# Kernel tuning notes

Hardware: AMD Instinct MI355X
Metric: run time of the kernel (lower is better)

The kernel has to match this reference:

```python
import jax, jax.numpy as jnp
import numpy as np

INV_SQRT2 = np.float32(1.0 / np.sqrt(2.0))


def _dwt1(x, axis):
    # pywt db1 (Haar), even-length: cA=(even+odd)/sqrt2, cD=(even-odd)/sqrt2
    ev = jax.lax.slice_in_dim(x, 0, None, 2, axis)
    od = jax.lax.slice_in_dim(x, 1, None, 2, axis)
    return (ev + od) * INV_SQRT2, (ev - od) * INV_SQRT2


def _idwt1(lo, hi, axis):
    ev = (lo + hi) * INV_SQRT2
    od = (lo - hi) * INV_SQRT2
    st = jnp.stack([ev, od], axis=axis + 1)  # (.., n, 2, ..)
    new_shape = list(lo.shape)
    new_shape[axis] *= 2
    return st.reshape(new_shape)


def haar_dwt2(x):
    lo, hi = _dwt1(x, 1)      # along width
    ll, lh = _dwt1(lo, 0)     # along height
    hl, hh = _dwt1(hi, 0)
    return ll, lh, hl, hh


def haar_idwt2(ll, lh, hl, hh):
    lo = _idwt1(ll, lh, 0)
    hi = _idwt1(hl, hh, 0)
    return _idwt1(lo, hi, 1)


def conv_same(img, w, b):
    # img: [h, w] -> 1x1-channel SAME conv with bias
    y = jax.lax.conv_general_dilated(
        img[None, None], w, (1, 1), 'SAME',
        dimension_numbers=('NCHW', 'OIHW', 'NCHW'))
    return y[0, 0] + b[0]


def setup_inputs() -> dict:
    key = jax.random.key(0)
    ks = jax.random.split(key, 7)
    H = W = 4096
    return {
        'x': jax.random.normal(ks[0], (1, 1, H, W), dtype=jnp.float32),
        'w3': jax.random.normal(ks[1], (1, 1, 3, 3), dtype=jnp.float32) * 0.1,
        'b3': jax.random.normal(ks[2], (1,), dtype=jnp.float32) * 0.1,
        'w5': jax.random.normal(ks[3], (1, 1, 5, 5), dtype=jnp.float32) * 0.1,
        'b5': jax.random.normal(ks[4], (1,), dtype=jnp.float32) * 0.1,
        'w7': jax.random.normal(ks[5], (1, 1, 7, 7), dtype=jnp.float32) * 0.1,
        'b7': jax.random.normal(ks[6], (1,), dtype=jnp.float32) * 0.1,
    }


def reference(x, w3, b3, w5, b5, w7, b7):
    img = x[0, 0]
    # 3-level wavedec2: collect details finest -> coarsest
    details = []
    cur = img
    for _ in range(3):
        ll, lh, hl, hh = haar_dwt2(cur)
        details.append((lh, hl, hh))
        cur = ll
    # pywt coeff order is coarsest-first, so in the torch code:
    # HH1 = coarsest (3x3), HH2 = mid (5x5), HH3 = finest (7x7)
    lh_c, hl_c, hh_c = details[2]
    lh_m, hl_m, hh_m = details[1]
    lh_f, hl_f, hh_f = details[0]
    hh_c = conv_same(hh_c, w3, b3)
    hh_m = conv_same(hh_m, w5, b5)
    hh_f = conv_same(hh_f, w7, b7)
    # waverec2: coarsest -> finest
    rec = haar_idwt2(cur, lh_c, hl_c, hh_c)
    rec = haar_idwt2(rec, lh_m, hl_m, hh_m)
    rec = haar_idwt2(rec, lh_f, hl_f, hh_f)
    return rec[None, None]
```

## Files before the change

### kernel.cpp

```cpp
#include <hip/hip_runtime.h>
#include <stddef.h>

#define IMG_N 4096

#define S_LH1   0
#define S_HL1   1680
#define S_HH1   3360
#define S_LL1   5040
#define S_HH1C  6720
#define S_LL2   7872
#define S_LH2   8272
#define S_HL2   8672
#define S_HH2   9072
#define S_LL2P  9472
#define S_LL3   9792
#define S_LH3   9892
#define S_HL3   9992
#define S_HH3   10092
#define S_TOTAL 10192

#define S_LL1P  (S_LL1)

__global__ __launch_bounds__(512, 8) void haar_fused(
    const float* __restrict__ x,
    const float* __restrict__ w3, const float* __restrict__ b3,
    const float* __restrict__ w5, const float* __restrict__ b5,
    const float* __restrict__ w7, const float* __restrict__ b7,
    float* __restrict__ out)
{
    __shared__ __align__(16) float sm[S_TOTAL];
    const int tid = threadIdx.x;
    const int bx = blockIdx.x, by = blockIdx.y;
    const int R0 = by * 64, C0 = bx * 64;

    float* LH1 = sm + S_LH1;
    float* HL1 = sm + S_HL1;
    float* HH1 = sm + S_HH1;
    float* LL1 = sm + S_LL1;
    float* HH1C = sm + S_HH1C;
    float* LL2 = sm + S_LL2;
    float* LH2 = sm + S_LH2;
    float* HL2 = sm + S_HL2;
    float* HH2 = sm + S_HH2;
    float* LL2P = sm + S_LL2P;
    float* LL3 = sm + S_LL3;
    float* LH3 = sm + S_LH3;
    float* HL3 = sm + S_HL3;
    float* HH3 = sm + S_HH3;
    float* LL1P = sm + S_LL1P;

    const bool interior = (by >= 1) && (by <= 62) && (bx >= 1) && (bx <= 62);
    if (interior) {
        const float* src = x + (size_t)(R0 - 8) * IMG_N + (C0 - 8);
        for (int idx = tid; idx < 800; idx += 512) {
            int u = idx / 20, v2 = (idx % 20) * 2;
            const float* p = src + (size_t)(2 * u) * IMG_N + 2 * v2;
            float4 t = *(const float4*)(p);
            float4 b = *(const float4*)(p + IMG_N);
            int o = u * 42 + v2;
            *(float2*)(LL1 + o) = make_float2((t.x + t.y + b.x + b.y) * 0.5f,
                                              (t.z + t.w + b.z + b.w) * 0.5f);
            *(float2*)(LH1 + o) = make_float2((t.x + t.y - b.x - b.y) * 0.5f,
                                              (t.z + t.w - b.z - b.w) * 0.5f);
            *(float2*)(HL1 + o) = make_float2((t.x - t.y + b.x - b.y) * 0.5f,
                                              (t.z - t.w + b.z - b.w) * 0.5f);
            *(float2*)(HH1 + o) = make_float2((t.x - t.y - b.x + b.y) * 0.5f,
                                              (t.z - t.w - b.z + b.w) * 0.5f);
        }
    } else {
        for (int idx = tid; idx < 800; idx += 512) {
            int u = idx / 20, v2 = (idx % 20) * 2;
            int gr0 = R0 - 8 + 2 * u, gr1 = gr0 + 1;
            int gc = C0 - 8 + 2 * v2;
            bool r0v = (gr0 >= 0 && gr0 < IMG_N), r1v = (gr1 >= 0 && gr1 < IMG_N);
            float tv[4], bv[4];
            #pragma unroll
            for (int k = 0; k < 4; ++k) {
                int g = gc + k;
                bool cv = (g >= 0 && g < IMG_N);
                tv[k] = (r0v && cv) ? x[(size_t)gr0 * IMG_N + g] : 0.0f;
                bv[k] = (r1v && cv) ? x[(size_t)gr1 * IMG_N + g] : 0.0f;
            }
            int o = u * 42 + v2;
            *(float2*)(LL1 + o) = make_float2((tv[0] + tv[1] + bv[0] + bv[1]) * 0.5f,
                                              (tv[2] + tv[3] + bv[2] + bv[3]) * 0.5f);
            *(float2*)(LH1 + o) = make_float2((tv[0] + tv[1] - bv[0] - bv[1]) * 0.5f,
                                              (tv[2] + tv[3] - bv[2] - bv[3]) * 0.5f);
            *(float2*)(HL1 + o) = make_float2((tv[0] - tv[1] + bv[0] - bv[1]) * 0.5f,
                                              (tv[2] - tv[3] + bv[2] - bv[3]) * 0.5f);
            *(float2*)(HH1 + o) = make_float2((tv[0] - tv[1] - bv[0] + bv[1]) * 0.5f,
                                              (tv[2] - tv[3] - bv[2] + bv[3]) * 0.5f);
        }
    }
    __syncthreads();

    if (tid < 256) {
        const int i = tid >> 3;
        const int j0 = (tid & 7) << 2;
        const float bias = b7[0];
        float a0 = bias, a1 = bias, a2 = bias, a3 = bias;
        #pragma unroll
        for (int dy = 0; dy < 7; ++dy) {
            const float* row = HH1 + (i + dy + 1) * 42 + (j0 + 1);
            const float* wr = w7 + dy * 7;
            float r0 = row[0], r1 = row[1], r2 = row[2], r3 = row[3], r4 = row[4],
                  r5 = row[5], r6 = row[6], r7 = row[7], r8 = row[8], r9 = row[9];
            float q0 = wr[0], q1 = wr[1], q2 = wr[2], q3 = wr[3], q4 = wr[4],
                  q5 = wr[5], q6 = wr[6];
            a0 += q0*r0 + q1*r1 + q2*r2 + q3*r3 + q4*r4 + q5*r5 + q6*r6;
            a1 += q0*r1 + q1*r2 + q2*r3 + q3*r4 + q4*r5 + q5*r6 + q6*r7;
            a2 += q0*r2 + q1*r3 + q2*r4 + q3*r5 + q4*r6 + q5*r7 + q6*r8;
            a3 += q0*r3 + q1*r4 + q2*r5 + q3*r6 + q4*r7 + q5*r8 + q6*r9;
        }
        *(float4*)(HH1C + i * 36 + j0) = make_float4(a0, a1, a2, a3);
    } else {
        int t = tid - 256;
        if (t < 200) {
            int u = t / 10, v2 = (t % 10) * 2;
            float4 tt = *(const float4*)(LL1 + (2 * u) * 42 + 2 * v2);
            float4 bb = *(const float4*)(LL1 + (2 * u + 1) * 42 + 2 * v2);
            int o = u * 20 + v2;
            *(float2*)(LL2 + o) = make_float2((tt.x + tt.y + bb.x + bb.y) * 0.5f,
                                              (tt.z + tt.w + bb.z + bb.w) * 0.5f);
            *(float2*)(LH2 + o) = make_float2((tt.x + tt.y - bb.x - bb.y) * 0.5f,
                                              (tt.z + tt.w - bb.z - bb.w) * 0.5f);
            *(float2*)(HL2 + o) = make_float2((tt.x - tt.y + bb.x - bb.y) * 0.5f,
                                              (tt.z - tt.w + bb.z - bb.w) * 0.5f);
            *(float2*)(HH2 + o) = make_float2((tt.x - tt.y - bb.x + bb.y) * 0.5f,
                                              (tt.z - tt.w - bb.z + bb.w) * 0.5f);
        }
    }
    __syncthreads();

    {
        int lane = tid & 63;
        if (lane < 50) {
            int u = lane / 5, v2 = (lane % 5) * 2;
            float4 tt = *(const float4*)(LL2 + (2 * u) * 20 + 2 * v2);
            float4 bb = *(const float4*)(LL2 + (2 * u + 1) * 20 + 2 * v2);
            int o = u * 10 + v2;
            *(float2*)(LL3 + o) = make_float2((tt.x + tt.y + bb.x + bb.y) * 0.5f,
                                              (tt.z + tt.w + bb.z + bb.w) * 0.5f);
            *(float2*)(LH3 + o) = make_float2((tt.x + tt.y - bb.x - bb.y) * 0.5f,
                                              (tt.z + tt.w - bb.z - bb.w) * 0.5f);
            *(float2*)(HL3 + o) = make_float2((tt.x - tt.y + bb.x - bb.y) * 0.5f,
                                              (tt.z - tt.w + bb.z - bb.w) * 0.5f);
            *(float2*)(HH3 + o) = make_float2((tt.x - tt.y - bb.x + bb.y) * 0.5f,
                                              (tt.z - tt.w - bb.z + bb.w) * 0.5f);
        }
        __builtin_amdgcn_wave_barrier();
        __builtin_amdgcn_s_waitcnt(0);
    }

    {
        const float b3c = b3[0];
        #pragma unroll
        for (int k = 0; k < 2; ++k) {
            int item = (tid & 63) + 64 * k;
            int p = item >> 3, c = item & 7;
            int r = p >> 1;
            float sr = (p & 1) ? -1.0f : 1.0f;
            float hh = b3c;
            #pragma unroll
            for (int dy = 0; dy < 3; ++dy) {
                const float* row = HH3 + (r + dy) * 10 + c;
                const float* wr = w3 + dy * 3;
                hh += wr[0]*row[0] + wr[1]*row[1] + wr[2]*row[2];
            }
            int li = (r + 1) * 10 + (c + 1);
            float lo = LL3[li] + sr * LH3[li];
            float hi = HL3[li] + sr * hh;
            *(float2*)(LL2P + p * 20 + 2 * c) =
                make_float2((lo + hi) * 0.5f, (lo - hi) * 0.5f);
        }
        __builtin_amdgcn_wave_barrier();
        __builtin_amdgcn_s_waitcnt(0);
    }

    {
        const float b5c = b5[0];
        int p = tid >> 4, c = tid & 15;
        int r = p >> 1;
        float sr = (p & 1) ? -1.0f : 1.0f;
        float hh = b5c;
        #pragma unroll
        for (int dy = 0; dy < 5; ++dy) {
            const float* row = HH2 + (r + dy) * 20 + c;
            const float* wr = w5 + dy * 5;
            hh += wr[0]*row[0] + wr[1]*row[1] + wr[2]*row[2] + wr[3]*row[3]
                + wr[4]*row[4];
        }
        int li = (r + 2) * 20 + (c + 2);
        float lo = LL2P[r * 20 + c] + sr * LH2[li];
        float hi = HL2[li] + sr * hh;
        *(float2*)(LL1P + p * 36 + 2 * c) =
            make_float2((lo + hi) * 0.5f, (lo - hi) * 0.5f);
    }
    __syncthreads();

    for (int idx = tid; idx < 1024; idx += 512) {
        const int p = idx >> 4;
        const int c2 = (idx & 15) * 2;
        const int r = p >> 1;
        const float sr = (p & 1) ? -1.0f : 1.0f;
        const int li = (r + 4) * 42 + (c2 + 4);
        const int ci = r * 36 + c2;
        float lo0 = LL1P[ci]     + sr * LH1[li];
        float hi0 = HL1[li]      + sr * HH1C[ci];
        float lo1 = LL1P[ci + 1] + sr * LH1[li + 1];
        float hi1 = HL1[li + 1]  + sr * HH1C[ci + 1];
        float4 o = make_float4((lo0 + hi0) * 0.5f, (lo0 - hi0) * 0.5f,
                               (lo1 + hi1) * 0.5f, (lo1 - hi1) * 0.5f);
        *(float4*)(out + (size_t)(R0 + p) * IMG_N + C0 + 2 * c2) = o;
    }
}

extern "C" void kernel_launch(void* const* d_in, const int* in_sizes, int n_in,
                              void* d_out, int out_size, void* d_ws, size_t ws_size,
                              hipStream_t stream) {
    (void)in_sizes; (void)n_in; (void)out_size; (void)d_ws; (void)ws_size;
    const float* x  = (const float*)d_in[0];
    const float* w3 = (const float*)d_in[1];
    const float* b3 = (const float*)d_in[2];
    const float* w5 = (const float*)d_in[3];
    const float* b5 = (const float*)d_in[4];
    const float* w7 = (const float*)d_in[5];
    const float* b7 = (const float*)d_in[6];
    float* out = (float*)d_out;

    dim3 grid(IMG_N / 64, IMG_N / 64);
    dim3 block(512);
    haar_fused<<<grid, block, 0, stream>>>(x, w3, b3, w5, b5, w7, b7, out);
}
```

Measured before the change: 142.3 us.

## Widen LDS rows to 44, vectorize Haar stages, precompute 5x5 conv, nontemporal stores

Pads first-level subband rows to 44 floats so every thread can load eight input columns with 2x float4 and write float4 results to LDS. The 7x7 conv reads rows as float4, and the level-2 split runs on 100 threads with float4 output. The 5x5 conv is moved into a separate stage that runs alongside the level-3 split, using shared-memory regions that are no longer needed. The final output is written with nontemporal stores. This adds one more __syncthreads and replaces the earlier wave-level barriers with block barriers.

```diff
diff --git a/kernel.cpp b/kernel.cpp
--- a/kernel.cpp
+++ b/kernel.cpp
@@ -3,23 +3,26 @@
 
 #define IMG_N 4096
 
+typedef float vf4 __attribute__((ext_vector_type(4)));
+
 #define S_LH1   0
-#define S_HL1   1680
-#define S_HH1   3360
-#define S_LL1   5040
-#define S_HH1C  6720
-#define S_LL2   7872
-#define S_LH2   8272
-#define S_HL2   8672
-#define S_HH2   9072
-#define S_LL2P  9472
-#define S_LL3   9792
-#define S_LH3   9892
-#define S_HL3   9992
-#define S_HH3   10092
-#define S_TOTAL 10192
-
+#define S_HL1   1760
+#define S_HH1   3520
+#define S_LL1   5280
+#define S_HH1C  7040
+#define S_LL2   8192
+#define S_LH2   8592
+#define S_HL2   8992
+#define S_HH2   9392
+#define S_TOTAL 9792
+
+#define S_HH2C  (S_HH1)
+#define S_LL3   (S_HH1 + 320)
+#define S_LH3   (S_HH1 + 420)
+#define S_HL3   (S_HH1 + 520)
+#define S_HH3   (S_HH1 + 620)
 #define S_LL1P  (S_LL1)
+#define S_LL2P  (S_LL1 + 1152)
 
 __global__ __launch_bounds__(512, 8) void haar_fused(
     const float* __restrict__ x,
@@ -33,64 +36,61 @@
     const int bx = blockIdx.x, by = blockIdx.y;
     const int R0 = by * 64, C0 = bx * 64;
 
-    float* LH1 = sm + S_LH1;
-    float* HL1 = sm + S_HL1;
-    float* HH1 = sm + S_HH1;
-    float* LL1 = sm + S_LL1;
+    float* LH1 = sm + S_LH1;   float* HL1 = sm + S_HL1;
+    float* HH1 = sm + S_HH1;   float* LL1 = sm + S_LL1;
     float* HH1C = sm + S_HH1C;
-    float* LL2 = sm + S_LL2;
-    float* LH2 = sm + S_LH2;
-    float* HL2 = sm + S_HL2;
-    float* HH2 = sm + S_HH2;
-    float* LL2P = sm + S_LL2P;
-    float* LL3 = sm + S_LL3;
-    float* LH3 = sm + S_LH3;
-    float* HL3 = sm + S_HL3;
-    float* HH3 = sm + S_HH3;
-    float* LL1P = sm + S_LL1P;
+    float* LL2 = sm + S_LL2;   float* LH2 = sm + S_LH2;
+    float* HL2 = sm + S_HL2;   float* HH2 = sm + S_HH2;
+    float* HH2C = sm + S_HH2C;
+    float* LL3 = sm + S_LL3;   float* LH3 = sm + S_LH3;
+    float* HL3 = sm + S_HL3;   float* HH3 = sm + S_HH3;
+    float* LL1P = sm + S_LL1P; float* LL2P = sm + S_LL2P;
 
     const bool interior = (by >= 1) && (by <= 62) && (bx >= 1) && (bx <= 62);
-    if (interior) {
-        const float* src = x + (size_t)(R0 - 8) * IMG_N + (C0 - 8);
-        for (int idx = tid; idx < 800; idx += 512) {
-            int u = idx / 20, v2 = (idx % 20) * 2;
-            const float* p = src + (size_t)(2 * u) * IMG_N + 2 * v2;
-            float4 t = *(const float4*)(p);
-            float4 b = *(const float4*)(p + IMG_N);
-            int o = u * 42 + v2;
-            *(float2*)(LL1 + o) = make_float2((t.x + t.y + b.x + b.y) * 0.5f,
-                                              (t.z + t.w + b.z + b.w) * 0.5f);
-            *(float2*)(LH1 + o) = make_float2((t.x + t.y - b.x - b.y) * 0.5f,
-                                              (t.z + t.w - b.z - b.w) * 0.5f);
-            *(float2*)(HL1 + o) = make_float2((t.x - t.y + b.x - b.y) * 0.5f,
-                                              (t.z - t.w + b.z - b.w) * 0.5f);
-            *(float2*)(HH1 + o) = make_float2((t.x - t.y - b.x + b.y) * 0.5f,
-                                              (t.z - t.w - b.z + b.w) * 0.5f);
-        }
-    } else {
-        for (int idx = tid; idx < 800; idx += 512) {
-            int u = idx / 20, v2 = (idx % 20) * 2;
-            int gr0 = R0 - 8 + 2 * u, gr1 = gr0 + 1;
-            int gc = C0 - 8 + 2 * v2;
-            bool r0v = (gr0 >= 0 && gr0 < IMG_N), r1v = (gr1 >= 0 && gr1 < IMG_N);
-            float tv[4], bv[4];
+    if (tid < 400) {
+        const int u = tid / 10, g = tid % 10;
+        float4 t0, t1, bb0, bb1;
+        if (interior) {
+            const float* p = x + (size_t)(R0 - 8 + 2 * u) * IMG_N + (C0 - 8 + 8 * g);
+            t0  = *(const float4*)(p);
+            t1  = *(const float4*)(p + 4);
+            bb0 = *(const float4*)(p + IMG_N);
+            bb1 = *(const float4*)(p + IMG_N + 4);
+        } else {
+            const int gr0 = R0 - 8 + 2 * u, gr1 = gr0 + 1;
+            const int gc = C0 - 8 + 8 * g;
+            const bool r0v = (gr0 >= 0 && gr0 < IMG_N), r1v = (gr1 >= 0 && gr1 < IMG_N);
+            float tv[8], bv[8];
             #pragma unroll
-            for (int k = 0; k < 4; ++k) {
-                int g = gc + k;
-                bool cv = (g >= 0 && g < IMG_N);
-                tv[k] = (r0v && cv) ? x[(size_t)gr0 * IMG_N + g] : 0.0f;
-                bv[k] = (r1v && cv) ? x[(size_t)gr1 * IMG_N + g] : 0.0f;
+            for (int k = 0; k < 8; ++k) {
+                int gck = gc + k;
+                bool cv = (gck >= 0 && gck < IMG_N);
+                tv[k] = (r0v && cv) ? x[(size_t)gr0 * IMG_N + gck] : 0.0f;
+                bv[k] = (r1v && cv) ? x[(size_t)gr1 * IMG_N + gck] : 0.0f;
             }
-            int o = u * 42 + v2;
-            *(float2*)(LL1 + o) = make_float2((tv[0] + tv[1] + bv[0] + bv[1]) * 0.5f,
-                                              (tv[2] + tv[3] + bv[2] + bv[3]) * 0.5f);
-            *(float2*)(LH1 + o) = make_float2((tv[0] + tv[1] - bv[0] - bv[1]) * 0.5f,
-                                              (tv[2] + tv[3] - bv[2] - bv[3]) * 0.5f);
-            *(float2*)(HL1 + o) = make_float2((tv[0] - tv[1] + bv[0] - bv[1]) * 0.5f,
-                                              (tv[2] - tv[3] + bv[2] - bv[3]) * 0.5f);
-            *(float2*)(HH1 + o) = make_float2((tv[0] - tv[1] - bv[0] + bv[1]) * 0.5f,
-                                              (tv[2] - tv[3] - bv[2] + bv[3]) * 0.5f);
-        }
+            t0  = make_float4(tv[0], tv[1], tv[2], tv[3]);
+            t1  = make_float4(tv[4], tv[5], tv[6], tv[7]);
+            bb0 = make_float4(bv[0], bv[1], bv[2], bv[3]);
+            bb1 = make_float4(bv[4], bv[5], bv[6], bv[7]);
+        }
+        float4 llv, lhv, hlv, hhv;
+        {
+            float a = t0.x, b = t0.y, c = bb0.x, d = bb0.y;
+            llv.x = (a + b + c + d) * 0.5f; lhv.x = (a + b - c - d) * 0.5f;
+            hlv.x = (a - b + c - d) * 0.5f; hhv.x = (a - b - c + d) * 0.5f;
+            a = t0.z; b = t0.w; c = bb0.z; d = bb0.w;
+            llv.y = (a + b + c + d) * 0.5f; lhv.y = (a + b - c - d) * 0.5f;
+            hlv.y = (a - b + c - d) * 0.5f; hhv.y = (a - b - c + d) * 0.5f;
+            a = t1.x; b = t1.y; c = bb1.x; d = bb1.y;
+            llv.z = (a + b + c + d) * 0.5f; lhv.z = (a + b - c - d) * 0.5f;
+            hlv.z = (a - b + c - d) * 0.5f; hhv.z = (a - b - c + d) * 0.5f;
+            a = t1.z; b = t1.w; c = bb1.z; d = bb1.w;
+            llv.w = (a + b + c + d) * 0.5f; lhv.w = (a + b - c - d) * 0.5f;
+            hlv.w = (a - b + c - d) * 0.5f; hhv.w = (a - b - c + d) * 0.5f;
+        }
+        const int o = u * 44 + 4 * g;
+        *(float4*)(LL1 + o) = llv;  *(float4*)(LH1 + o) = lhv;
+        *(float4*)(HL1 + o) = hlv;  *(float4*)(HH1 + o) = hhv;
     }
     __syncthreads();
 
@@ -101,117 +101,128 @@
         float a0 = bias, a1 = bias, a2 = bias, a3 = bias;
         #pragma unroll
         for (int dy = 0; dy < 7; ++dy) {
-            const float* row = HH1 + (i + dy + 1) * 42 + (j0 + 1);
+            const float* rp = HH1 + (i + dy + 1) * 44 + j0;
+            float4 A = *(const float4*)(rp);
+            float4 B = *(const float4*)(rp + 4);
+            float4 C = *(const float4*)(rp + 8);
             const float* wr = w7 + dy * 7;
-            float r0 = row[0], r1 = row[1], r2 = row[2], r3 = row[3], r4 = row[4],
-                  r5 = row[5], r6 = row[6], r7 = row[7], r8 = row[8], r9 = row[9];
             float q0 = wr[0], q1 = wr[1], q2 = wr[2], q3 = wr[3], q4 = wr[4],
                   q5 = wr[5], q6 = wr[6];
-            a0 += q0*r0 + q1*r1 + q2*r2 + q3*r3 + q4*r4 + q5*r5 + q6*r6;
-            a1 += q0*r1 + q1*r2 + q2*r3 + q3*r4 + q4*r5 + q5*r6 + q6*r7;
-            a2 += q0*r2 + q1*r3 + q2*r4 + q3*r5 + q4*r6 + q5*r7 + q6*r8;
-            a3 += q0*r3 + q1*r4 + q2*r5 + q3*r6 + q4*r7 + q5*r8 + q6*r9;
+            a0 += q0*A.y + q1*A.z + q2*A.w + q3*B.x + q4*B.y + q5*B.z + q6*B.w;
+            a1 += q0*A.z + q1*A.w + q2*B.x + q3*B.y + q4*B.z + q5*B.w + q6*C.x;
+            a2 += q0*A.w + q1*B.x + q2*B.y + q3*B.z + q4*B.w + q5*C.x + q6*C.y;
+            a3 += q0*B.x + q1*B.y + q2*B.z + q3*B.w + q4*C.x + q5*C.y + q6*C.z;
         }
         *(float4*)(HH1C + i * 36 + j0) = make_float4(a0, a1, a2, a3);
-    } else {
-        int t = tid - 256;
-        if (t < 200) {
-            int u = t / 10, v2 = (t % 10) * 2;
-            float4 tt = *(const float4*)(LL1 + (2 * u) * 42 + 2 * v2);
-            float4 bb = *(const float4*)(LL1 + (2 * u + 1) * 42 + 2 * v2);
-            int o = u * 20 + v2;
-            *(float2*)(LL2 + o) = make_float2((tt.x + tt.y + bb.x + bb.y) * 0.5f,
-                                              (tt.z + tt.w + bb.z + bb.w) * 0.5f);
-            *(float2*)(LH2 + o) = make_float2((tt.x + tt.y - bb.x - bb.y) * 0.5f,
-                                              (tt.z + tt.w - bb.z - bb.w) * 0.5f);
-            *(float2*)(HL2 + o) = make_float2((tt.x - tt.y + bb.x - bb.y) * 0.5f,
-                                              (tt.z - tt.w + bb.z - bb.w) * 0.5f);
-            *(float2*)(HH2 + o) = make_float2((tt.x - tt.y - bb.x + bb.y) * 0.5f,
-                                              (tt.z - tt.w - bb.z + bb.w) * 0.5f);
-        }
-    }
-    __syncthreads();
-
-    {
-        int lane = tid & 63;
-        if (lane < 50) {
-            int u = lane / 5, v2 = (lane % 5) * 2;
-            float4 tt = *(const float4*)(LL2 + (2 * u) * 20 + 2 * v2);
-            float4 bb = *(const float4*)(LL2 + (2 * u + 1) * 20 + 2 * v2);
-            int o = u * 10 + v2;
-            *(float2*)(LL3 + o) = make_float2((tt.x + tt.y + bb.x + bb.y) * 0.5f,
-                                              (tt.z + tt.w + bb.z + bb.w) * 0.5f);
-            *(float2*)(LH3 + o) = make_float2((tt.x + tt.y - bb.x - bb.y) * 0.5f,
-                                              (tt.z + tt.w - bb.z - bb.w) * 0.5f);
-            *(float2*)(HL3 + o) = make_float2((tt.x - tt.y + bb.x - bb.y) * 0.5f,
-                                              (tt.z - tt.w + bb.z - bb.w) * 0.5f);
-            *(float2*)(HH3 + o) = make_float2((tt.x - tt.y - bb.x + bb.y) * 0.5f,
-                                              (tt.z - tt.w - bb.z + bb.w) * 0.5f);
-        }
-        __builtin_amdgcn_wave_barrier();
-        __builtin_amdgcn_s_waitcnt(0);
-    }
-
-    {
-        const float b3c = b3[0];
-        #pragma unroll
-        for (int k = 0; k < 2; ++k) {
-            int item = (tid & 63) + 64 * k;
-            int p = item >> 3, c = item & 7;
-            int r = p >> 1;
-            float sr = (p & 1) ? -1.0f : 1.0f;
-            float hh = b3c;
-            #pragma unroll
-            for (int dy = 0; dy < 3; ++dy) {
-                const float* row = HH3 + (r + dy) * 10 + c;
-                const float* wr = w3 + dy * 3;
-                hh += wr[0]*row[0] + wr[1]*row[1] + wr[2]*row[2];
-            }
-            int li = (r + 1) * 10 + (c + 1);
-            float lo = LL3[li] + sr * LH3[li];
-            float hi = HL3[li] + sr * hh;
-            *(float2*)(LL2P + p * 20 + 2 * c) =
-                make_float2((lo + hi) * 0.5f, (lo - hi) * 0.5f);
-        }
-        __builtin_amdgcn_wave_barrier();
-        __builtin_amdgcn_s_waitcnt(0);
-    }
-
-    {
-        const float b5c = b5[0];
-        int p = tid >> 4, c = tid & 15;
-        int r = p >> 1;
-        float sr = (p & 1) ? -1.0f : 1.0f;
-        float hh = b5c;
+    } else if (tid < 356) {
+        const int t = tid - 256;
+        const int u = t / 5, g = t % 5;
+        const float* rp = LL1 + (2 * u) * 44 + 8 * g;
+        float4 t0 = *(const float4*)(rp),      t1 = *(const float4*)(rp + 4);
+        float4 c0 = *(const float4*)(rp + 44), c1 = *(const float4*)(rp + 48);
+        float4 llv, lhv, hlv, hhv;
+        llv.x = (t0.x + t0.y + c0.x + c0.y) * 0.5f; lhv.x = (t0.x + t0.y - c0.x - c0.y) * 0.5f;
+        hlv.x = (t0.x - t0.y + c0.x - c0.y) * 0.5f; hhv.x = (t0.x - t0.y - c0.x + c0.y) * 0.5f;
+        llv.y = (t0.z + t0.w + c0.z + c0.w) * 0.5f; lhv.y = (t0.z + t0.w - c0.z - c0.w) * 0.5f;
+        hlv.y = (t0.z - t0.w + c0.z - c0.w) * 0.5f; hhv.y = (t0.z - t0.w - c0.z + c0.w) * 0.5f;
+        llv.z = (t1.x + t1.y + c1.x + c1.y) * 0.5f; lhv.z = (t1.x + t1.y - c1.x - c1.y) * 0.5f;
+        hlv.z = (t1.x - t1.y + c1.x - c1.y) * 0.5f; hhv.z = (t1.x - t1.y - c1.x + c1.y) * 0.5f;
+        llv.w = (t1.z + t1.w + c1.z + c1.w) * 0.5f; lhv.w = (t1.z + t1.w - c1.z - c1.w) * 0.5f;
+        hlv.w = (t1.z - t1.w + c1.z - c1.w) * 0.5f; hhv.w = (t1.z - t1.w - c1.z + c1.w) * 0.5f;
+        const int o = u * 20 + 4 * g;
+        *(float4*)(LL2 + o) = llv;  *(float4*)(LH2 + o) = lhv;
+        *(float4*)(HL2 + o) = hlv;  *(float4*)(HH2 + o) = hhv;
+    }
+    __syncthreads();
+
+    if (tid < 50) {
+        const int u = tid / 5, v2 = (tid % 5) * 2;
+        const float* rp = LL2 + (2 * u) * 20 + 2 * v2;
+        float4 t0 = *(const float4*)(rp);
+        float4 c0 = *(const float4*)(rp + 20);
+        const int o = u * 10 + v2;
+        *(float2*)(LL3 + o) = make_float2((t0.x + t0.y + c0.x + c0.y) * 0.5f,
+                                          (t0.z + t0.w + c0.z + c0.w) * 0.5f);
+        *(float2*)(LH3 + o) = make_float2((t0.x + t0.y - c0.x - c0.y) * 0.5f,
+                                          (t0.z + t0.w - c0.z - c0.w) * 0.5f);
+        *(float2*)(HL3 + o) = make_float2((t0.x - t0.y + c0.x - c0.y) * 0.5f,
+                                          (t0.z - t0.w + c0.z - c0.w) * 0.5f);
+        *(float2*)(HH3 + o) = make_float2((t0.x - t0.y - c0.x + c0.y) * 0.5f,
+                                          (t0.z - t0.w - c0.z + c0.w) * 0.5f);
+    } else if (tid >= 64 && tid < 128) {
+        const int s = tid - 64;
+        const int i = s >> 2;
+        const int j0 = (s & 3) << 2;
+        const float bias = b5[0];
+        float a0 = bias, a1 = bias, a2 = bias, a3 = bias;
         #pragma unroll
         for (int dy = 0; dy < 5; ++dy) {
-            const float* row = HH2 + (r + dy) * 20 + c;
+            const float* rp = HH2 + (i + dy) * 20 + j0;
+            float4 A = *(const float4*)(rp);
+            float4 B = *(const float4*)(rp + 4);
             const float* wr = w5 + dy * 5;
-            hh += wr[0]*row[0] + wr[1]*row[1] + wr[2]*row[2] + wr[3]*row[3]
-                + wr[4]*row[4];
-        }
-        int li = (r + 2) * 20 + (c + 2);
+            float q0 = wr[0], q1 = wr[1], q2 = wr[2], q3 = wr[3], q4 = wr[4];
+            a0 += q0*A.x + q1*A.y + q2*A.z + q3*A.w + q4*B.x;
+            a1 += q0*A.y + q1*A.z + q2*A.w + q3*B.x + q4*B.y;
+            a2 += q0*A.z + q1*A.w + q2*B.x + q3*B.y + q4*B.z;
+            a3 += q0*A.w + q1*B.x + q2*B.y + q3*B.z + q4*B.w;
+        }
+        *(float4*)(HH2C + i * 20 + j0) = make_float4(a0, a1, a2, a3);
+    }
+    __syncthreads();
+
+    if (tid < 128) {
+        const int p = tid >> 3, c = tid & 7;
+        const int r = p >> 1;
+        const float sr = (p & 1) ? -1.0f : 1.0f;
+        float hh = b3[0];
+        #pragma unroll
+        for (int dy = 0; dy < 3; ++dy) {
+            const float* row = HH3 + (r + dy) * 10 + c;
+            const float* wr = w3 + dy * 3;
+            hh += wr[0]*row[0] + wr[1]*row[1] + wr[2]*row[2];
+        }
+        const int li = (r + 1) * 10 + (c + 1);
+        float lo = LL3[li] + sr * LH3[li];
+        float hi = HL3[li] + sr * hh;
+        *(float2*)(LL2P + p * 20 + 2 * c) =
+            make_float2((lo + hi) * 0.5f, (lo - hi) * 0.5f);
+    }
+    __syncthreads();
+
+    {
+        const int p = tid >> 4, c = tid & 15;
+        const int r = p >> 1;
+        const float sr = (p & 1) ? -1.0f : 1.0f;
+        const int li = (r + 2) * 20 + (c + 2);
         float lo = LL2P[r * 20 + c] + sr * LH2[li];
-        float hi = HL2[li] + sr * hh;
+        float hi = HL2[li] + sr * HH2C[r * 20 + c];
         *(float2*)(LL1P + p * 36 + 2 * c) =
             make_float2((lo + hi) * 0.5f, (lo - hi) * 0.5f);
     }
     __syncthreads();
 
-    for (int idx = tid; idx < 1024; idx += 512) {
+    #pragma unroll
+    for (int k = 0; k < 2; ++k) {
+        const int idx = tid + 512 * k;
         const int p = idx >> 4;
         const int c2 = (idx & 15) * 2;
         const int r = p >> 1;
         const float sr = (p & 1) ? -1.0f : 1.0f;
-        const int li = (r + 4) * 42 + (c2 + 4);
+        const int li = (r + 4) * 44 + (c2 + 4);
         const int ci = r * 36 + c2;
-        float lo0 = LL1P[ci]     + sr * LH1[li];
-        float hi0 = HL1[li]      + sr * HH1C[ci];
-        float lo1 = LL1P[ci + 1] + sr * LH1[li + 1];
-        float hi1 = HL1[li + 1]  + sr * HH1C[ci + 1];
-        float4 o = make_float4((lo0 + hi0) * 0.5f, (lo0 - hi0) * 0.5f,
-                               (lo1 + hi1) * 0.5f, (lo1 - hi1) * 0.5f);
-        *(float4*)(out + (size_t)(R0 + p) * IMG_N + C0 + 2 * c2) = o;
+        float2 llp = *(const float2*)(LL1P + ci);
+        float2 lh  = *(const float2*)(LH1 + li);
+        float2 hl  = *(const float2*)(HL1 + li);
+        float2 hhc = *(const float2*)(HH1C + ci);
+        float lo0 = llp.x + sr * lh.x;
+        float hi0 = hl.x + sr * hhc.x;
+        float lo1 = llp.y + sr * lh.y;
+        float hi1 = hl.y + sr * hhc.y;
+        vf4 o = { (lo0 + hi0) * 0.5f, (lo0 - hi0) * 0.5f,
+                  (lo1 + hi1) * 0.5f, (lo1 - hi1) * 0.5f };
+        __builtin_nontemporal_store(
+            o, (vf4*)(out + (size_t)(R0 + p) * IMG_N + C0 + 2 * c2));
     }
 }
 
```

Result: faster. 133.4 us (-6.3%).
